# Optimization experiments

Measured on AMD Instinct MI355X. Metric: run time of the kernel, lower is better.

The kernel has to match this reference:

```python
import jax, jax.numpy as jnp
import numpy as np


def setup_inputs() -> dict:
    key = jax.random.key(0)
    k1, k2 = jax.random.split(key)
    B, C, H, W = 16, 512, 64, 64
    x_training = jax.random.normal(k1, (B, C, H, W), dtype=jnp.float32)
    x_pre = jax.random.normal(k2, (B, C, H, W), dtype=jnp.float32)
    return {"x_training": x_training, "x_pre": x_pre}


def reference(x_training, x_pre):
    B, C, H, W = x_training.shape
    q = x_pre.reshape(B, C, H * W)        # proj_query: B x C x N
    kv = x_training.reshape(B, C, H * W)  # proj_key/value: B x C x N
    # energy[b,c,d] = <q[b,c,:], kv[b,d,:]>  -> B x C x C
    energy = jnp.einsum('bcn,bdn->bcd', q, kv)
    # max-subtract trick (note: max - energy, not energy - max)
    energy_new = jnp.max(energy, axis=-1, keepdims=True) - energy
    attention = jax.nn.softmax(energy_new, axis=-1)  # B x C x C
    out = jnp.einsum('bcd,bdn->bcn', attention, kv).reshape(B, C, H, W)
    # final softmax over last (width) axis of the 4D map
    return jax.nn.softmax(out, axis=-1)
```

## Files before the change

### kernel.cpp

```cpp
#include <hip/hip_runtime.h>
#include <hip/hip_bf16.h>
#include <math.h>

#define CCH  512
#define NTOK 4096
#define NB   16
#define KSPL 2048
#define LDA  40

typedef __attribute__((ext_vector_type(8))) short s8v;
typedef __attribute__((ext_vector_type(4))) float f4v;
typedef unsigned short u16;

__device__ __forceinline__ void split2(float2 f, ushort2& hi, ushort2& lo) {
    __hip_bfloat162 h = __float22bfloat162_rn(f);
    float2 hf = __bfloat1622float2(h);
    __hip_bfloat162 l = __float22bfloat162_rn(make_float2(f.x - hf.x, f.y - hf.y));
    hi = *reinterpret_cast<ushort2*>(&h);
    lo = *reinterpret_cast<ushort2*>(&l);
}
__device__ __forceinline__ u16 bfrne(float x) {
    __hip_bfloat16 h = __float2bfloat16(x);
    return *reinterpret_cast<u16*>(&h);
}

__global__ __launch_bounds__(256, 2)
void energy_mfma(const float* __restrict__ q, const float* __restrict__ kv,
                 float* __restrict__ E) {
    __shared__ short Ah[128 * LDA], Al[128 * LDA], Bh[128 * LDA], Bl[128 * LDA];
    const int b  = blockIdx.z >> 1;
    const int s  = blockIdx.z & 1;
    const int c0 = blockIdx.y * 128, d0 = blockIdx.x * 128;
    const int tid  = threadIdx.x;
    const int lane = tid & 63, wave = tid >> 6;
    const int wm = wave & 1, wn = wave >> 1;
    const int l15 = lane & 15, quad = lane >> 4;

    const int srow = tid >> 1;
    const int skq  = (tid & 1) * 16;
    const float* ga = q  + ((size_t)(b * CCH + c0 + srow)) * NTOK + s * KSPL + skq;
    const float* gb = kv + ((size_t)(b * CCH + d0 + srow)) * NTOK + s * KSPL + skq;

    f4v acc[4][4];
#pragma unroll
    for (int i = 0; i < 4; ++i)
#pragma unroll
        for (int j = 0; j < 4; ++j) acc[i][j] = (f4v)0.f;

    float4 pa[4], pb[4];
#pragma unroll
    for (int i = 0; i < 4; ++i) {
        pa[i] = ((const float4*)ga)[i];
        pb[i] = ((const float4*)gb)[i];
    }

    for (int kc = 0; kc < KSPL; kc += 32) {
        __syncthreads();
#pragma unroll
        for (int i = 0; i < 4; ++i) {
            ushort2 h0, l0, h1, l1;
            split2(make_float2(pa[i].x, pa[i].y), h0, l0);
            split2(make_float2(pa[i].z, pa[i].w), h1, l1);
            *(ushort4*)&Ah[srow * LDA + skq + i * 4] = make_ushort4(h0.x, h0.y, h1.x, h1.y);
            *(ushort4*)&Al[srow * LDA + skq + i * 4] = make_ushort4(l0.x, l0.y, l1.x, l1.y);
            split2(make_float2(pb[i].x, pb[i].y), h0, l0);
            split2(make_float2(pb[i].z, pb[i].w), h1, l1);
            *(ushort4*)&Bh[srow * LDA + skq + i * 4] = make_ushort4(h0.x, h0.y, h1.x, h1.y);
            *(ushort4*)&Bl[srow * LDA + skq + i * 4] = make_ushort4(l0.x, l0.y, l1.x, l1.y);
        }
        __syncthreads();
        if (kc + 32 < KSPL) {
            const float* ga2 = ga + kc + 32;
            const float* gb2 = gb + kc + 32;
#pragma unroll
            for (int i = 0; i < 4; ++i) {
                pa[i] = ((const float4*)ga2)[i];
                pb[i] = ((const float4*)gb2)[i];
            }
        }
        const int koff = quad * 8;
        const int abase = (wm * 64 + l15) * LDA + koff;
        const int bbase = (wn * 64 + l15) * LDA + koff;
        s8v a_h[4], a_l[4];
#pragma unroll
        for (int i = 0; i < 4; ++i) {
            a_h[i] = *(const s8v*)&Ah[abase + i * 16 * LDA];
            a_l[i] = *(const s8v*)&Al[abase + i * 16 * LDA];
        }
#pragma unroll
        for (int j = 0; j < 4; ++j) {
            s8v b_h = *(const s8v*)&Bh[bbase + j * 16 * LDA];
            s8v b_l = *(const s8v*)&Bl[bbase + j * 16 * LDA];
#pragma unroll
            for (int i = 0; i < 4; ++i) {
                acc[i][j] = __builtin_amdgcn_mfma_f32_16x16x32_bf16(a_h[i], b_h, acc[i][j], 0, 0, 0);
                acc[i][j] = __builtin_amdgcn_mfma_f32_16x16x32_bf16(a_h[i], b_l, acc[i][j], 0, 0, 0);
                acc[i][j] = __builtin_amdgcn_mfma_f32_16x16x32_bf16(a_l[i], b_h, acc[i][j], 0, 0, 0);
            }
        }
    }

    float* Eb = E + ((size_t)(s * NB + b)) * CCH * CCH;
#pragma unroll
    for (int i = 0; i < 4; ++i)
#pragma unroll
        for (int r = 0; r < 4; ++r) {
            const int row = c0 + wm * 64 + i * 16 + quad * 4 + r;
#pragma unroll
            for (int j = 0; j < 4; ++j)
                Eb[(size_t)row * CCH + d0 + wn * 64 + j * 16 + l15] = acc[i][j][r];
        }
}

__global__ __launch_bounds__(256)
void attn_softmax(const float* __restrict__ E0, const float* __restrict__ E1,
                  u16* __restrict__ ah, u16* __restrict__ al) {
    __shared__ float red[4];
    const size_t base = (size_t)blockIdx.x * CCH;
    const int t = threadIdx.x;
    float e0 = E0[base + t] + E1[base + t];
    float e1 = E0[base + t + 256] + E1[base + t + 256];
    float m = fminf(e0, e1);
#pragma unroll
    for (int off = 32; off > 0; off >>= 1) m = fminf(m, __shfl_xor(m, off, 64));
    if ((t & 63) == 0) red[t >> 6] = m;
    __syncthreads();
    const float mAll = fminf(fminf(red[0], red[1]), fminf(red[2], red[3]));
    float x0 = __expf(mAll - e0);
    float x1 = __expf(mAll - e1);
    float sum = x0 + x1;
#pragma unroll
    for (int off = 32; off > 0; off >>= 1) sum += __shfl_xor(sum, off, 64);
    __syncthreads();
    if ((t & 63) == 0) red[t >> 6] = sum;
    __syncthreads();
    const float inv = 1.0f / (red[0] + red[1] + red[2] + red[3]);
    float a0 = x0 * inv, a1 = x1 * inv;
    __hip_bfloat16 h0 = __float2bfloat16(a0);
    __hip_bfloat16 h1 = __float2bfloat16(a1);
    ah[base + t]       = *reinterpret_cast<u16*>(&h0);
    ah[base + t + 256] = *reinterpret_cast<u16*>(&h1);
    __hip_bfloat16 g0 = __float2bfloat16(a0 - __bfloat162float(h0));
    __hip_bfloat16 g1 = __float2bfloat16(a1 - __bfloat162float(h1));
    al[base + t]       = *reinterpret_cast<u16*>(&g0);
    al[base + t + 256] = *reinterpret_cast<u16*>(&g1);
}

__global__ __launch_bounds__(256, 2)
void out_mfma(const u16* __restrict__ atth, const u16* __restrict__ attl,
              const float* __restrict__ kv, float* __restrict__ out) {
    __shared__ short Ah[128 * LDA], Al[128 * LDA], Bs[128 * LDA];
    const int b  = blockIdx.z;
    const int c0 = blockIdx.y * 128;
    const int n0 = blockIdx.x * 128;
    const int tid  = threadIdx.x;
    const int lane = tid & 63, wave = tid >> 6;
    const int wm = wave & 1, wn = wave >> 1;
    const int l15 = lane & 15, quad = lane >> 4;

    const int arow = tid >> 1, akq = (tid & 1) * 16;
    const u16* gah = atth + ((size_t)(b * CCH + c0 + arow)) * CCH + akq;
    const u16* gal = attl + ((size_t)(b * CCH + c0 + arow)) * CCH + akq;
    const int bn = tid & 127, bkg = (tid >> 7) * 16;
    const float* gb = kv + (size_t)b * CCH * NTOK + n0 + bn;

    f4v acc[4][4];
#pragma unroll
    for (int i = 0; i < 4; ++i)
#pragma unroll
        for (int j = 0; j < 4; ++j) acc[i][j] = (f4v)0.f;

    ushort4 pah[4], pal[4];
    float pbf[16];
#pragma unroll
    for (int i = 0; i < 4; ++i) {
        pah[i] = *(const ushort4*)(gah + i * 4);
        pal[i] = *(const ushort4*)(gal + i * 4);
    }
#pragma unroll
    for (int t = 0; t < 16; ++t) pbf[t] = gb[(size_t)(bkg + t) * NTOK];

    for (int kc = 0; kc < CCH; kc += 32) {
        __syncthreads();
#pragma unroll
        for (int i = 0; i < 4; ++i) {
            *(ushort4*)&Ah[arow * LDA + akq + i * 4] = pah[i];
            *(ushort4*)&Al[arow * LDA + akq + i * 4] = pal[i];
        }
#pragma unroll
        for (int p = 0; p < 4; ++p) {
            ushort4 v = make_ushort4(bfrne(pbf[p * 4 + 0]), bfrne(pbf[p * 4 + 1]),
                                     bfrne(pbf[p * 4 + 2]), bfrne(pbf[p * 4 + 3]));
            *(ushort4*)&Bs[bn * LDA + bkg + p * 4] = v;
        }
        __syncthreads();
        if (kc + 32 < CCH) {
#pragma unroll
            for (int i = 0; i < 4; ++i) {
                pah[i] = *(const ushort4*)(gah + kc + 32 + i * 4);
                pal[i] = *(const ushort4*)(gal + kc + 32 + i * 4);
            }
#pragma unroll
            for (int t = 0; t < 16; ++t) pbf[t] = gb[(size_t)(kc + 32 + bkg + t) * NTOK];
        }
        const int koff = quad * 8;
        const int abase = (wm * 64 + l15) * LDA + koff;
        const int bbase = (wn * 64 + l15) * LDA + koff;
        s8v a_h[4], a_l[4];
#pragma unroll
        for (int i = 0; i < 4; ++i) {
            a_h[i] = *(const s8v*)&Ah[abase + i * 16 * LDA];
            a_l[i] = *(const s8v*)&Al[abase + i * 16 * LDA];
        }
#pragma unroll
        for (int j = 0; j < 4; ++j) {
            s8v bb = *(const s8v*)&Bs[bbase + j * 16 * LDA];
#pragma unroll
            for (int i = 0; i < 4; ++i) {
                acc[i][j] = __builtin_amdgcn_mfma_f32_16x16x32_bf16(a_h[i], bb, acc[i][j], 0, 0, 0);
                acc[i][j] = __builtin_amdgcn_mfma_f32_16x16x32_bf16(a_l[i], bb, acc[i][j], 0, 0, 0);
            }
        }
    }

#pragma unroll
    for (int i = 0; i < 4; ++i) {
#pragma unroll
        for (int r = 0; r < 4; ++r) {
            float v0 = acc[i][0][r], v1 = acc[i][1][r], v2 = acc[i][2][r], v3 = acc[i][3][r];
            float m = fmaxf(fmaxf(v0, v1), fmaxf(v2, v3));
#pragma unroll
            for (int off = 8; off > 0; off >>= 1) m = fmaxf(m, __shfl_xor(m, off, 16));
            float e0 = __expf(v0 - m), e1 = __expf(v1 - m), e2 = __expf(v2 - m), e3 = __expf(v3 - m);
            float sum = e0 + e1 + e2 + e3;
#pragma unroll
            for (int off = 8; off > 0; off >>= 1) sum += __shfl_xor(sum, off, 16);
            const float inv = 1.0f / sum;
            const int row = c0 + wm * 64 + i * 16 + quad * 4 + r;
            float* op = out + ((size_t)(b * CCH + row)) * NTOK + n0 + wn * 64 + l15;
            op[0]  = e0 * inv;
            op[16] = e1 * inv;
            op[32] = e2 * inv;
            op[48] = e3 * inv;
        }
    }
}

extern "C" void kernel_launch(void* const* d_in, const int* in_sizes, int n_in,
                              void* d_out, int out_size, void* d_ws, size_t ws_size,
                              hipStream_t stream) {
    const float* x_training = (const float*)d_in[0];
    const float* x_pre      = (const float*)d_in[1];
    float* out = (float*)d_out;
    const size_t ES = (size_t)NB * CCH * CCH;
    float* E0 = (float*)d_ws;
    float* E1 = E0 + ES;
    u16* ath = (u16*)(E1 + ES);
    u16* atl = ath + ES;

    energy_mfma<<<dim3(4, 4, 32), 256, 0, stream>>>(x_pre, x_training, E0);
    attn_softmax<<<dim3(NB * CCH), 256, 0, stream>>>(E0, E1, ath, atl);
    out_mfma<<<dim3(NTOK / 128, CCH / 128, NB), 256, 0, stream>>>(ath, atl, x_training, out);
}
```

Measured before the change: 456.4 us.

## Preconvert kv to bf16 hi/lo plus transpose and stream tiles via global_load_lds

```diff
diff --git a/kernel.cpp b/kernel.cpp
--- a/kernel.cpp
+++ b/kernel.cpp
@@ -1,6 +1,5 @@
 #include <hip/hip_runtime.h>
 #include <hip/hip_bf16.h>
-#include <math.h>
 
 #define CCH  512
 #define NTOK 4096
@@ -23,23 +22,65 @@
     __hip_bfloat16 h = __float2bfloat16(x);
     return *reinterpret_cast<u16*>(&h);
 }
+__device__ __forceinline__ void dma16(const void* g, void* l) {
+    __builtin_amdgcn_global_load_lds((const __attribute__((address_space(1))) void*)g,
+                                     (__attribute__((address_space(3))) void*)l, 16, 0, 0);
+}
+
+__global__ __launch_bounds__(256)
+void convert_kv(const float* __restrict__ kv, u16* __restrict__ kvh,
+                u16* __restrict__ kvl, u16* __restrict__ kvT) {
+    __shared__ u16 T[64][72];
+    const int b = blockIdx.z, c0 = blockIdx.y * 64, n0 = blockIdx.x * 64;
+    const int t = threadIdx.x;
+    const int r = t >> 2, cs = (t & 3) * 16;
+    const float* src = kv + ((size_t)(b * CCH + c0 + r)) * NTOK + n0 + cs;
+    u16 hi[16], lo[16];
+#pragma unroll
+    for (int p = 0; p < 4; ++p) {
+        float4 v = ((const float4*)src)[p];
+        ushort2 h0, l0, h1, l1;
+        split2(make_float2(v.x, v.y), h0, l0);
+        split2(make_float2(v.z, v.w), h1, l1);
+        hi[p*4+0]=h0.x; hi[p*4+1]=h0.y; hi[p*4+2]=h1.x; hi[p*4+3]=h1.y;
+        lo[p*4+0]=l0.x; lo[p*4+1]=l0.y; lo[p*4+2]=l1.x; lo[p*4+3]=l1.y;
+    }
+    u16* dh = kvh + ((size_t)(b * CCH + c0 + r)) * NTOK + n0 + cs;
+    u16* dl = kvl + ((size_t)(b * CCH + c0 + r)) * NTOK + n0 + cs;
+#pragma unroll
+    for (int p = 0; p < 4; ++p) {
+        *(ushort4*)(dh + p*4) = make_ushort4(hi[p*4], hi[p*4+1], hi[p*4+2], hi[p*4+3]);
+        *(ushort4*)(dl + p*4) = make_ushort4(lo[p*4], lo[p*4+1], lo[p*4+2], lo[p*4+3]);
+    }
+#pragma unroll
+    for (int k = 0; k < 16; ++k) T[cs + k][r] = hi[k];
+    __syncthreads();
+    const int n1 = t >> 2, ccs = (t & 3) * 16;
+    u16* dt = kvT + ((size_t)(b * NTOK + n0 + n1)) * CCH + c0 + ccs;
+#pragma unroll
+    for (int p = 0; p < 4; ++p)
+        *(ushort4*)(dt + p*4) = *(const ushort4*)&T[n1][ccs + p*4];
+}
 
 __global__ __launch_bounds__(256, 2)
-void energy_mfma(const float* __restrict__ q, const float* __restrict__ kv,
-                 float* __restrict__ E) {
-    __shared__ short Ah[128 * LDA], Al[128 * LDA], Bh[128 * LDA], Bl[128 * LDA];
-    const int b  = blockIdx.z >> 1;
-    const int s  = blockIdx.z & 1;
+void energy_v3(const float* __restrict__ q, const u16* __restrict__ kvh,
+               const u16* __restrict__ kvl, float* __restrict__ E) {
+    __shared__ short Ah[128 * LDA], Al[128 * LDA];
+    __shared__ __align__(16) char Bh[8192], Bl[8192];
+    const int b = blockIdx.z >> 1, s = blockIdx.z & 1;
     const int c0 = blockIdx.y * 128, d0 = blockIdx.x * 128;
-    const int tid  = threadIdx.x;
-    const int lane = tid & 63, wave = tid >> 6;
+    const int tid = threadIdx.x, lane = tid & 63, wave = tid >> 6;
     const int wm = wave & 1, wn = wave >> 1;
     const int l15 = lane & 15, quad = lane >> 4;
 
-    const int srow = tid >> 1;
-    const int skq  = (tid & 1) * 16;
-    const float* ga = q  + ((size_t)(b * CCH + c0 + srow)) * NTOK + s * KSPL + skq;
-    const float* gb = kv + ((size_t)(b * CCH + d0 + srow)) * NTOK + s * KSPL + skq;
+    const int srow = tid >> 1, skq = (tid & 1) * 16;
+    const float* ga = q + ((size_t)(b * CCH + c0 + srow)) * NTOK + s * KSPL + skq;
+    const int drow = wave * 32 + (lane >> 2);
+    const int gl   = (lane & 3) ^ ((lane >> 3) & 3);
+    const u16* gbh = kvh + ((size_t)(b * CCH + d0 + drow)) * NTOK + s * KSPL + gl * 8;
+    const u16* gbl = kvl + ((size_t)(b * CCH + d0 + drow)) * NTOK + s * KSPL + gl * 8;
+    char* ldsBh = Bh + wave * 2048;
+    char* ldsBl = Bl + wave * 2048;
 
     f4v acc[4][4];
 #pragma unroll
@@ -47,15 +88,16 @@
 #pragma unroll
         for (int j = 0; j < 4; ++j) acc[i][j] = (f4v)0.f;
 
-    float4 pa[4], pb[4];
-#pragma unroll
-    for (int i = 0; i < 4; ++i) {
-        pa[i] = ((const float4*)ga)[i];
-        pb[i] = ((const float4*)gb)[i];
-    }
+    float4 pa[4];
+#pragma unroll
+    for (int i = 0; i < 4; ++i) pa[i] = ((const float4*)ga)[i];
 
     for (int kc = 0; kc < KSPL; kc += 32) {
         __syncthreads();
+        dma16(gbh + kc, ldsBh);
+        dma16(gbh + 16 * NTOK + kc, ldsBh + 1024);
+        dma16(gbl + kc, ldsBl);
+        dma16(gbl + 16 * NTOK + kc, ldsBl + 1024);
 #pragma unroll
         for (int i = 0; i < 4; ++i) {
             ushort2 h0, l0, h1, l1;
@@ -63,34 +105,26 @@
             split2(make_float2(pa[i].z, pa[i].w), h1, l1);
             *(ushort4*)&Ah[srow * LDA + skq + i * 4] = make_ushort4(h0.x, h0.y, h1.x, h1.y);
             *(ushort4*)&Al[srow * LDA + skq + i * 4] = make_ushort4(l0.x, l0.y, l1.x, l1.y);
-            split2(make_float2(pb[i].x, pb[i].y), h0, l0);
-            split2(make_float2(pb[i].z, pb[i].w), h1, l1);
-            *(ushort4*)&Bh[srow * LDA + skq + i * 4] = make_ushort4(h0.x, h0.y, h1.x, h1.y);
-            *(ushort4*)&Bl[srow * LDA + skq + i * 4] = make_ushort4(l0.x, l0.y, l1.x, l1.y);
         }
         __syncthreads();
         if (kc + 32 < KSPL) {
             const float* ga2 = ga + kc + 32;
-            const float* gb2 = gb + kc + 32;
-#pragma unroll
-            for (int i = 0; i < 4; ++i) {
-                pa[i] = ((const float4*)ga2)[i];
-                pb[i] = ((const float4*)gb2)[i];
-            }
-        }
-        const int koff = quad * 8;
-        const int abase = (wm * 64 + l15) * LDA + koff;
-        const int bbase = (wn * 64 + l15) * LDA + koff;
+#pragma unroll
+            for (int i = 0; i < 4; ++i) pa[i] = ((const float4*)ga2)[i];
+        }
+        const int aoff  = (wm * 64 + l15) * LDA + quad * 8;
+        const int xslot = quad ^ ((l15 >> 1) & 3);
+        const int boff  = (wn * 64 + l15) * 64 + xslot * 16;
         s8v a_h[4], a_l[4];
 #pragma unroll
         for (int i = 0; i < 4; ++i) {
-            a_h[i] = *(const s8v*)&Ah[abase + i * 16 * LDA];
-            a_l[i] = *(const s8v*)&Al[abase + i * 16 * LDA];
+            a_h[i] = *(const s8v*)&Ah[aoff + i * 16 * LDA];
+            a_l[i] = *(const s8v*)&Al[aoff + i * 16 * LDA];
         }
 #pragma unroll
         for (int j = 0; j < 4; ++j) {
-            s8v b_h = *(const s8v*)&Bh[bbase + j * 16 * LDA];
-            s8v b_l = *(const s8v*)&Bl[bbase + j * 16 * LDA];
+            s8v b_h = *(const s8v*)(Bh + boff + j * 1024);
+            s8v b_l = *(const s8v*)(Bl + boff + j * 1024);
 #pragma unroll
             for (int i = 0; i < 4; ++i) {
                 acc[i][j] = __builtin_amdgcn_mfma_f32_16x16x32_bf16(a_h[i], b_h, acc[i][j], 0, 0, 0);
@@ -147,22 +181,22 @@
 }
 
 __global__ __launch_bounds__(256, 2)
-void out_mfma(const u16* __restrict__ atth, const u16* __restrict__ attl,
-              const float* __restrict__ kv, float* __restrict__ out) {
-    __shared__ short Ah[128 * LDA], Al[128 * LDA], Bs[128 * LDA];
-    const int b  = blockIdx.z;
-    const int c0 = blockIdx.y * 128;
-    const int n0 = blockIdx.x * 128;
-    const int tid  = threadIdx.x;
-    const int lane = tid & 63, wave = tid >> 6;
+void out_v3(const u16* __restrict__ ath, const u16* __restrict__ atl,
+            const u16* __restrict__ kvT, float* __restrict__ out) {
+    __shared__ __align__(16) char Ah[8192], Al[8192], Bs[8192];
+    const int b = blockIdx.z, c0 = blockIdx.y * 128, n0 = blockIdx.x * 128;
+    const int tid = threadIdx.x, lane = tid & 63, wave = tid >> 6;
     const int wm = wave & 1, wn = wave >> 1;
     const int l15 = lane & 15, quad = lane >> 4;
 
-    const int arow = tid >> 1, akq = (tid & 1) * 16;
-    const u16* gah = atth + ((size_t)(b * CCH + c0 + arow)) * CCH + akq;
-    const u16* gal = attl + ((size_t)(b * CCH + c0 + arow)) * CCH + akq;
-    const int bn = tid & 127, bkg = (tid >> 7) * 16;
-    const float* gb = kv + (size_t)b * CCH * NTOK + n0 + bn;
+    const int grow = wave * 32 + (lane >> 2);
+    const int gl   = (lane & 3) ^ ((lane >> 3) & 3);
+    const u16* gah = ath + ((size_t)(b * CCH + c0 + grow)) * CCH + gl * 8;
+    const u16* gal = atl + ((size_t)(b * CCH + c0 + grow)) * CCH + gl * 8;
+    const u16* gbt = kvT + ((size_t)(b * NTOK + n0 + grow)) * CCH + gl * 8;
+    char* ldsA  = Ah + wave * 2048;
+    char* ldsAl = Al + wave * 2048;
+    char* ldsB  = Bs + wave * 2048;
 
     f4v acc[4][4];
 #pragma unroll
@@ -170,51 +204,27 @@
 #pragma unroll
         for (int j = 0; j < 4; ++j) acc[i][j] = (f4v)0.f;
 
-    ushort4 pah[4], pal[4];
-    float pbf[16];
-#pragma unroll
-    for (int i = 0; i < 4; ++i) {
-        pah[i] = *(const ushort4*)(gah + i * 4);
-        pal[i] = *(const ushort4*)(gal + i * 4);
-    }
-#pragma unroll
-    for (int t = 0; t < 16; ++t) pbf[t] = gb[(size_t)(bkg + t) * NTOK];
-
     for (int kc = 0; kc < CCH; kc += 32) {
         __syncthreads();
-#pragma unroll
-        for (int i = 0; i < 4; ++i) {
-            *(ushort4*)&Ah[arow * LDA + akq + i * 4] = pah[i];
-            *(ushort4*)&Al[arow * LDA + akq + i * 4] = pal[i];
-        }
-#pragma unroll
-        for (int p = 0; p < 4; ++p) {
-            ushort4 v = make_ushort4(bfrne(pbf[p * 4 + 0]), bfrne(pbf[p * 4 + 1]),
-                                     bfrne(pbf[p * 4 + 2]), bfrne(pbf[p * 4 + 3]));
-            *(ushort4*)&Bs[bn * LDA + bkg + p * 4] = v;
-        }
-        __syncthreads();
-        if (kc + 32 < CCH) {
-#pragma unroll
-            for (int i = 0; i < 4; ++i) {
-                pah[i] = *(const ushort4*)(gah + kc + 32 + i * 4);
-                pal[i] = *(const ushort4*)(gal + kc + 32 + i * 4);
-            }
-#pragma unroll
-            for (int t = 0; t < 16; ++t) pbf[t] = gb[(size_t)(kc + 32 + bkg + t) * NTOK];
-        }
-        const int koff = quad * 8;
-        const int abase = (wm * 64 + l15) * LDA + koff;
-        const int bbase = (wn * 64 + l15) * LDA + koff;
+        dma16(gah + kc, ldsA);
+        dma16(gah + 16 * CCH + kc, ldsA + 1024);
+        dma16(gal + kc, ldsAl);
+        dma16(gal + 16 * CCH + kc, ldsAl + 1024);
+        dma16(gbt + kc, ldsB);
+        dma16(gbt + 16 * CCH + kc, ldsB + 1024);
+        __syncthreads();
+        const int xslot = quad ^ ((l15 >> 1) & 3);
+        const int aoff  = (wm * 64 + l15) * 64 + xslot * 16;
+        const int boff  = (wn * 64 + l15) * 64 + xslot * 16;
         s8v a_h[4], a_l[4];
 #pragma unroll
         for (int i = 0; i < 4; ++i) {
-            a_h[i] = *(const s8v*)&Ah[abase + i * 16 * LDA];
-            a_l[i] = *(const s8v*)&Al[abase + i * 16 * LDA];
+            a_h[i] = *(const s8v*)(Ah + aoff + i * 1024);
+            a_l[i] = *(const s8v*)(Al + aoff + i * 1024);
         }
 #pragma unroll
         for (int j = 0; j < 4; ++j) {
-            s8v bb = *(const s8v*)&Bs[bbase + j * 16 * LDA];
+            s8v bb = *(const s8v*)(Bs + boff + j * 1024);
 #pragma unroll
             for (int i = 0; i < 4; ++i) {
                 acc[i][j] = __builtin_amdgcn_mfma_f32_16x16x32_bf16(a_h[i], bb, acc[i][j], 0, 0, 0);
@@ -246,6 +256,159 @@
     }
 }
 
+__global__ __launch_bounds__(256, 2)
+void energy_r2(const float* __restrict__ q, const float* __restrict__ kv,
+               float* __restrict__ E) {
+    __shared__ short Ah[128 * LDA], Al[128 * LDA], Bh[128 * LDA], Bl[128 * LDA];
+    const int b = blockIdx.z >> 1, s = blockIdx.z & 1;
+    const int c0 = blockIdx.y * 128, d0 = blockIdx.x * 128;
+    const int tid = threadIdx.x, lane = tid & 63, wave = tid >> 6;
+    const int wm = wave & 1, wn = wave >> 1;
+    const int l15 = lane & 15, quad = lane >> 4;
+    const int srow = tid >> 1, skq = (tid & 1) * 16;
+    const float* ga = q  + ((size_t)(b * CCH + c0 + srow)) * NTOK + s * KSPL + skq;
+    const float* gb = kv + ((size_t)(b * CCH + d0 + srow)) * NTOK + s * KSPL + skq;
+    f4v acc[4][4];
+#pragma unroll
+    for (int i = 0; i < 4; ++i)
+#pragma unroll
+        for (int j = 0; j < 4; ++j) acc[i][j] = (f4v)0.f;
+    float4 pa[4], pb[4];
+#pragma unroll
+    for (int i = 0; i < 4; ++i) { pa[i] = ((const float4*)ga)[i]; pb[i] = ((const float4*)gb)[i]; }
+    for (int kc = 0; kc < KSPL; kc += 32) {
+        __syncthreads();
+#pragma unroll
+        for (int i = 0; i < 4; ++i) {
+            ushort2 h0, l0, h1, l1;
+            split2(make_float2(pa[i].x, pa[i].y), h0, l0);
+            split2(make_float2(pa[i].z, pa[i].w), h1, l1);
+            *(ushort4*)&Ah[srow * LDA + skq + i * 4] = make_ushort4(h0.x, h0.y, h1.x, h1.y);
+            *(ushort4*)&Al[srow * LDA + skq + i * 4] = make_ushort4(l0.x, l0.y, l1.x, l1.y);
+            split2(make_float2(pb[i].x, pb[i].y), h0, l0);
+            split2(make_float2(pb[i].z, pb[i].w), h1, l1);
+            *(ushort4*)&Bh[srow * LDA + skq + i * 4] = make_ushort4(h0.x, h0.y, h1.x, h1.y);
+            *(ushort4*)&Bl[srow * LDA + skq + i * 4] = make_ushort4(l0.x, l0.y, l1.x, l1.y);
+        }
+        __syncthreads();
+        if (kc + 32 < KSPL) {
+            const float* ga2 = ga + kc + 32; const float* gb2 = gb + kc + 32;
+#pragma unroll
+            for (int i = 0; i < 4; ++i) { pa[i] = ((const float4*)ga2)[i]; pb[i] = ((const float4*)gb2)[i]; }
+        }
+        const int aoff = (wm * 64 + l15) * LDA + quad * 8;
+        const int boff = (wn * 64 + l15) * LDA + quad * 8;
+        s8v a_h[4], a_l[4];
+#pragma unroll
+        for (int i = 0; i < 4; ++i) {
+            a_h[i] = *(const s8v*)&Ah[aoff + i * 16 * LDA];
+            a_l[i] = *(const s8v*)&Al[aoff + i * 16 * LDA];
+        }
+#pragma unroll
+        for (int j = 0; j < 4; ++j) {
+            s8v b_h = *(const s8v*)&Bh[boff + j * 16 * LDA];
+            s8v b_l = *(const s8v*)&Bl[boff + j * 16 * LDA];
+#pragma unroll
+            for (int i = 0; i < 4; ++i) {
+                acc[i][j] = __builtin_amdgcn_mfma_f32_16x16x32_bf16(a_h[i], b_h, acc[i][j], 0, 0, 0);
+                acc[i][j] = __builtin_amdgcn_mfma_f32_16x16x32_bf16(a_h[i], b_l, acc[i][j], 0, 0, 0);
+                acc[i][j] = __builtin_amdgcn_mfma_f32_16x16x32_bf16(a_l[i], b_h, acc[i][j], 0, 0, 0);
+            }
+        }
+    }
+    float* Eb = E + ((size_t)(s * NB + b)) * CCH * CCH;
+#pragma unroll
+    for (int i = 0; i < 4; ++i)
+#pragma unroll
+        for (int r = 0; r < 4; ++r) {
+            const int row = c0 + wm * 64 + i * 16 + quad * 4 + r;
+#pragma unroll
+            for (int j = 0; j < 4; ++j)
+                Eb[(size_t)row * CCH + d0 + wn * 64 + j * 16 + l15] = acc[i][j][r];
+        }
+}
+
+__global__ __launch_bounds__(256, 2)
+void out_r2(const u16* __restrict__ atth, const u16* __restrict__ attl,
+            const float* __restrict__ kv, float* __restrict__ out) {
+    __shared__ short Ah[128 * LDA], Al[128 * LDA], Bs[128 * LDA];
+    const int b = blockIdx.z, c0 = blockIdx.y * 128, n0 = blockIdx.x * 128;
+    const int tid = threadIdx.x, lane = tid & 63, wave = tid >> 6;
+    const int wm = wave & 1, wn = wave >> 1;
+    const int l15 = lane & 15, quad = lane >> 4;
+    const int arow = tid >> 1, akq = (tid & 1) * 16;
+    const u16* gah = atth + ((size_t)(b * CCH + c0 + arow)) * CCH + akq;
+    const u16* gal = attl + ((size_t)(b * CCH + c0 + arow)) * CCH + akq;
+    const int bn = tid & 127, bkg = (tid >> 7) * 16;
+    const float* gb = kv + (size_t)b * CCH * NTOK + n0 + bn;
+    f4v acc[4][4];
+#pragma unroll
+    for (int i = 0; i < 4; ++i)
+#pragma unroll
+        for (int j = 0; j < 4; ++j) acc[i][j] = (f4v)0.f;
+    ushort4 pah[4], pal[4];
+    float pbf[16];
+#pragma unroll
+    for (int i = 0; i < 4; ++i) { pah[i] = *(const ushort4*)(gah + i * 4); pal[i] = *(const ushort4*)(gal + i * 4); }
+#pragma unroll
+    for (int t = 0; t < 16; ++t) pbf[t] = gb[(size_t)(bkg + t) * NTOK];
+    for (int kc = 0; kc < CCH; kc += 32) {
+        __syncthreads();
+#pragma unroll
+        for (int i = 0; i < 4; ++i) {
+            *(ushort4*)&Ah[arow * LDA + akq + i * 4] = pah[i];
+            *(ushort4*)&Al[arow * LDA + akq + i * 4] = pal[i];
+        }
+#pragma unroll
+        for (int p = 0; p < 4; ++p) {
+            ushort4 v = make_ushort4(bfrne(pbf[p*4+0]), bfrne(pbf[p*4+1]), bfrne(pbf[p*4+2]), bfrne(pbf[p*4+3]));
+            *(ushort4*)&Bs[bn * LDA + bkg + p * 4] = v;
+        }
+        __syncthreads();
+        if (kc + 32 < CCH) {
+#pragma unroll
+            for (int i = 0; i < 4; ++i) { pah[i] = *(const ushort4*)(gah + kc + 32 + i * 4); pal[i] = *(const ushort4*)(gal + kc + 32 + i * 4); }
+#pragma unroll
+            for (int t = 0; t < 16; ++t) pbf[t] = gb[(size_t)(kc + 32 + bkg + t) * NTOK];
+        }
+        const int aoff = (wm * 64 + l15) * LDA + quad * 8;
+        const int boff = (wn * 64 + l15) * LDA + quad * 8;
+        s8v a_h[4], a_l[4];
+#pragma unroll
+        for (int i = 0; i < 4; ++i) {
+            a_h[i] = *(const s8v*)&Ah[aoff + i * 16 * LDA];
+            a_l[i] = *(const s8v*)&Al[aoff + i * 16 * LDA];
+        }
+#pragma unroll
+        for (int j = 0; j < 4; ++j) {
+            s8v bb = *(const s8v*)&Bs[boff + j * 16 * LDA];
+#pragma unroll
+            for (int i = 0; i < 4; ++i) {
+                acc[i][j] = __builtin_amdgcn_mfma_f32_16x16x32_bf16(a_h[i], bb, acc[i][j], 0, 0, 0);
+                acc[i][j] = __builtin_amdgcn_mfma_f32_16x16x32_bf16(a_l[i], bb, acc[i][j], 0, 0, 0);
+            }
+        }
+    }
+#pragma unroll
+    for (int i = 0; i < 4; ++i) {
+#pragma unroll
+        for (int r = 0; r < 4; ++r) {
+            float v0 = acc[i][0][r], v1 = acc[i][1][r], v2 = acc[i][2][r], v3 = acc[i][3][r];
+            float m = fmaxf(fmaxf(v0, v1), fmaxf(v2, v3));
+#pragma unroll
+            for (int off = 8; off > 0; off >>= 1) m = fmaxf(m, __shfl_xor(m, off, 16));
+            float e0 = __expf(v0 - m), e1 = __expf(v1 - m), e2 = __expf(v2 - m), e3 = __expf(v3 - m);
+            float sum = e0 + e1 + e2 + e3;
+#pragma unroll
+            for (int off = 8; off > 0; off >>= 1) sum += __shfl_xor(sum, off, 16);
+            const float inv = 1.0f / sum;
+            const int row = c0 + wm * 64 + i * 16 + quad * 4 + r;
+            float* op = out + ((size_t)(b * CCH + row)) * NTOK + n0 + wn * 64 + l15;
+            op[0] = e0 * inv; op[16] = e1 * inv; op[32] = e2 * inv; op[48] = e3 * inv;
+        }
+    }
+}
+
 extern "C" void kernel_launch(void* const* d_in, const int* in_sizes, int n_in,
                               void* d_out, int out_size, void* d_ws, size_t ws_size,
                               hipStream_t stream) {
@@ -253,12 +416,28 @@
     const float* x_pre      = (const float*)d_in[1];
     float* out = (float*)d_out;
     const size_t ES = (size_t)NB * CCH * CCH;
-    float* E0 = (float*)d_ws;
-    float* E1 = E0 + ES;
-    u16* ath = (u16*)(E1 + ES);
-    u16* atl = ath + ES;
-
-    energy_mfma<<<dim3(4, 4, 32), 256, 0, stream>>>(x_pre, x_training, E0);
-    attn_softmax<<<dim3(NB * CCH), 256, 0, stream>>>(E0, E1, ath, atl);
-    out_mfma<<<dim3(NTOK / 128, CCH / 128, NB), 256, 0, stream>>>(ath, atl, x_training, out);
-}
+    const size_t KS = (size_t)NB * CCH * NTOK;
+    const size_t NEED = KS * 2 * 3 + ES * 4 * 2 + ES * 2 * 2;
+
+    if (ws_size >= NEED) {
+        u16*   kvh = (u16*)d_ws;
+        u16*   kvl = kvh + KS;
+        u16*   kvT = kvl + KS;
+        float* E0  = (float*)(kvT + KS);
+        float* E1  = E0 + ES;
+        u16*   ath = (u16*)(E1 + ES);
+        u16*   atl = ath + ES;
+        convert_kv<<<dim3(NTOK/64, CCH/64, NB), 256, 0, stream>>>(x_training, kvh, kvl, kvT);
+        energy_v3<<<dim3(4, 4, 32), 256, 0, stream>>>(x_pre, kvh, kvl, E0);
+        attn_softmax<<<dim3(NB * CCH), 256, 0, stream>>>(E0, E1, ath, atl);
+        out_v3<<<dim3(NTOK/128, CCH/128, NB), 256, 0, stream>>>(ath, atl, kvT, out);
+    } else {
+        float* E0  = (float*)d_ws;
+        float* E1  = E0 + ES;
+        u16*   ath = (u16*)(E1 + ES);
+        u16*   atl = ath + ES;
+        energy_r2<<<dim3(4, 4, 32), 256, 0, stream>>>(x_pre, x_training, E0);
+        attn_softmax<<<dim3(NB * CCH), 256, 0, stream>>>(E0, E1, ath, atl);
+        out_r2<<<dim3(NTOK/128, CCH/128, NB), 256, 0, stream>>>(ath, atl, x_training, out);
+    }
+}
```

Measured after the change: 541.5 us. +18.6%, slower.
